# Kernel optimization log

Hardware: AMD Instinct MI355X
Metric: run time of the kernel (lower is better)

Reference implementation:

```python
import math
import jax, jax.numpy as jnp
import numpy as np

# ---- static hyperparams (match init_kwargs) ----
B, D, K, NC, F = 16384, 64, 128, 64, 256
TAU_MIN = 0.01
TAU_DENOM_MIN = 0.001
EPS = 0.001  # transport_eps


def setup_inputs() -> dict:
    key = jax.random.key(0)
    ks = jax.random.split(key, 8)
    # latent positions strictly inside the Poincare ball (norm < 0.9)
    z = jax.random.normal(ks[0], (B, D), jnp.float32)
    z = z / (jnp.linalg.norm(z, axis=-1, keepdims=True) + 1e-6)
    z = z * (0.9 * jax.random.uniform(ks[1], (B, 1), jnp.float32))
    features = jax.random.normal(ks[2], (B, F), jnp.float32)
    q_z_w = jax.random.normal(ks[3], (K, D), jnp.float32) * 0.02
    q_z_b = jnp.zeros((K,), jnp.float32)
    q_feat_w = jax.random.normal(ks[4], (K, F), jnp.float32) * 0.02
    q_feat_b = jnp.zeros((K,), jnp.float32)
    q_gamma = jax.random.normal(ks[5], (K, D, D), jnp.float32) * 0.02
    chart_queries = jax.random.normal(ks[6], (NC, K), jnp.float32) * 0.02
    return {"z": z, "features": features, "q_z_w": q_z_w, "q_z_b": q_z_b,
            "q_feat_w": q_feat_w, "q_feat_b": q_feat_b, "q_gamma": q_gamma,
            "chart_queries": chart_queries}


def _hyperbolic_score(z, centers):
    # z: [B, D]; centers: [NC, D] -> scores [B, NC]
    diff = z[:, None, :] - centers[None, :, :]
    dist_sq = (diff ** 2).sum(-1)                       # [B, NC]
    z_sq = (z ** 2).sum(-1, keepdims=True)              # [B, 1]
    c_sq = (centers ** 2).sum(-1)[None, :]              # [1, NC]
    denom = (1.0 - z_sq) * (1.0 - c_sq)
    arg = 1.0 + 2.0 * dist_sq / (denom + EPS)
    dist = jnp.arccosh(jnp.maximum(arg, 1.0 + EPS))
    # metric-aware temperature tau(z)
    tau = math.sqrt(K) * jnp.maximum(1.0 - z_sq[:, 0], TAU_DENOM_MIN) / 2.0
    tau = jnp.maximum(tau, TAU_MIN)                     # [B]
    return -dist / tau[:, None]


def reference(z, features, q_z_w, q_z_b, q_feat_w, q_feat_b, q_gamma, chart_queries):
    # chart centers live in the first D coords of the chart queries
    centers = chart_queries[:, :D]                      # [NC, D]
    scores = _hyperbolic_score(z, centers)              # [B, NC]

    # query: linear(z) + linear(features) + bilinear gamma term
    q = z @ q_z_w.T + q_z_b + features @ q_feat_w.T + q_feat_b   # [B, K]
    q = q + jnp.einsum("bi,bj,kij->bk", z, z, q_gamma)           # gamma contraction

    # O(n) hyperbolic parallel transport: scale queries by 1/lambda(z)
    r2 = jnp.minimum((z ** 2).sum(-1, keepdims=True), 1.0 - EPS)  # [B, 1]
    lam = 2.0 / (1.0 - r2 + EPS)                                  # [B, 1]
    tq = chart_queries[None, :, :] / lam[:, None, :]              # [B, NC, K]

    scores = scores + jnp.einsum("bk,bnk->bn", q, tq) / math.sqrt(K)
    weights = jax.nn.softmax(scores, axis=-1)           # [B, NC] (soft routing)
    k_chart = jnp.argmax(weights, axis=-1)              # [B]
    return weights, k_chart
```

## Files before the change

### kernel.cpp

```cpp
#include <hip/hip_runtime.h>
#include <hip/hip_bf16.h>
#include <cmath>
#include <cstring>

#define B_TOT 16384

typedef unsigned int uint_t;
typedef unsigned short ushort_t;
typedef __attribute__((ext_vector_type(8))) short bf16x8;
typedef __attribute__((ext_vector_type(16))) float f32x16;

#define WS_TAB 0
#define WS_CSQ 1024
#define WS_LIN 4096
#define WS_S   4198400
#define WS_PPK 5246976

__global__ __launch_bounds__(256) void prep_s(const float* __restrict__ g,
                                              const float* __restrict__ cq,
                                              char* __restrict__ ws) {
  __shared__ float gl[128][68];
  __shared__ float cql[16][132];
  float* S = (float*)(ws + WS_S);
  const int ns = blockIdx.x >> 6, J = blockIdx.x & 63, t = threadIdx.x;
  for (int i = t; i < 2048; i += 256) {
    const int k = i >> 4, c4 = (i & 15) * 4;
    *(float4*)&gl[k][c4] = *(const float4*)(g + (size_t)k * 4096 + J * 64 + c4);
  }
  for (int i = t; i < 2048; i += 256) {
    const int n16 = i >> 7, k = i & 127;
    cql[n16][k] = cq[(ns * 16 + n16) * 128 + k];
  }
  __syncthreads();
  const int n16 = t >> 4, c4 = (t & 15) * 4;
  float4 acc = {0.f, 0.f, 0.f, 0.f};
#pragma unroll 8
  for (int k = 0; k < 128; ++k) {
    const float w = cql[n16][k];
    const float4 gv = *(const float4*)&gl[k][c4];
    acc.x = fmaf(w, gv.x, acc.x);
    acc.y = fmaf(w, gv.y, acc.y);
    acc.z = fmaf(w, gv.z, acc.z);
    acc.w = fmaf(w, gv.w, acc.w);
  }
  *(float4*)(S + (size_t)(ns * 16 + n16) * 4096 + J * 64 + c4) = acc;
}

__global__ __launch_bounds__(256) void prep_pack(
    const float* __restrict__ qfw, const float* __restrict__ cq,
    const float* __restrict__ qzw, const float* __restrict__ qzb,
    const float* __restrict__ qfb, char* __restrict__ ws) {
  __shared__ float Sl[4096];
  __shared__ uint_t tabl[192];
  __shared__ float psumf[128][2];
  const int n = blockIdx.x & 63, part = blockIdx.x >> 6, t = threadIdx.x;
  const float* __restrict__ S = (const float*)(ws + WS_S) + (size_t)n * 4096;
  for (int i = t; i < 4096; i += 256) Sl[i] = S[i];
  if (t < 64) {
    const int i = t;
    const int start = (i < 16) ? 4 * i
                     : (i < 32) ? 64 + 3 * (i - 16)
                     : (i < 48) ? 112 + 2 * (i - 32)
                                : 144 + (i - 48);
    const int nst = 4 - (i >> 4);
    for (int u = 0; u < nst; ++u)
      tabl[start + u] = (0u << 16) | ((uint_t)i << 8) | (uint_t)(16 * ((i >> 4) + u));
  } else if (t < 80) tabl[160 + (t - 64)] = (1u << 16) | (uint_t)((t - 64) * 16);
  else if (t < 84)   tabl[176 + (t - 80)] = (2u << 16) | (uint_t)((t - 80) * 16);
  else if (t == 84)  tabl[180] = (3u << 16);
  else if (t < 96)   tabl[181 + (t - 85)] = 0;
  __syncthreads();
  if (part == 0 && n == 0 && t < 192) ((uint_t*)(ws + WS_TAB))[t] = tabl[t];

  const int mt = n >> 5, r = n & 31;
  auto wpack = [&](int s, int jo, float val) {
    const __hip_bfloat16 hb = __float2bfloat16(val);
    const float hf = __bfloat162float(hb);
    const __hip_bfloat16 lb = __float2bfloat16(val - hf);
    ushort_t hu, lu;
    memcpy(&hu, &hb, 2);
    memcpy(&lu, &lb, 2);
    const size_t base =
        (((size_t)s * 4 + mt * 2) * 64 + ((jo >> 3) & 1) * 32 + r) * 16 + (jo & 7) * 2;
    *(ushort_t*)(ws + WS_PPK + base) = hu;
    *(ushort_t*)(ws + WS_PPK + base + 1024) = lu;
  };

  for (int v = part * 640 + t; v < (part + 1) * 640; v += 256) {
    const int s = v >> 4, jo = v & 15;
    const uint_t inf = tabl[s];
    const int i = (inf >> 8) & 255, j0 = inf & 255;
    const int j = j0 + jo;
    const float val =
        (j < i) ? 0.f : ((j > i) ? Sl[i * 64 + j] + Sl[j * 64 + i] : Sl[i * 64 + i]);
    wpack(s, jo, val);
  }
  const float* __restrict__ cqn = cq + n * 128;

  if (part >= 2) {
    const int fl = t & 127, kh = t >> 7;
    const int f = (part - 2) * 128 + fl;
    float a = 0.f;
#pragma unroll 8
    for (int k = 0; k < 64; ++k)
      a = fmaf(qfw[(kh * 64 + k) * 256 + f], cqn[kh * 64 + k], a);
    psumf[fl][kh] = a;
    __syncthreads();
    if (t < 128) {
      const int ff = (part - 2) * 128 + t;
      wpack(160 + (ff >> 4), ff & 15, psumf[t][0] + psumf[t][1]);
    }
  } else if (part == 1) {
    if (t < 64) {
      float a = 0.f;
#pragma unroll 8
      for (int k = 0; k < 128; ++k) a = fmaf(cqn[k], qzw[k * 64 + t], a);
      wpack(176 + (t >> 4), t & 15, a);
    }
    for (int v2 = t; v2 < 176; v2 += 256) wpack(181 + (v2 >> 4), v2 & 15, 0.f);
  } else {
    if (t == 128) {
      float a = 0.f;
      for (int k = 0; k < 128; ++k) a = fmaf(qzb[k] + qfb[k], cqn[k], a);
      wpack(180, 0, a);
    } else if (t > 128 && t < 144) wpack(180, t - 128, 0.f);
    if (t == 144) {
      double a = 0.0;
      for (int d = 0; d < 64; ++d) a = fma((double)cqn[d], (double)cqn[d], a);
      ((double*)(ws + WS_CSQ))[n] = a;
    }
  }
}

__global__ __launch_bounds__(256, 4) void gemm_tail_kernel(
    const float* __restrict__ z, const float* __restrict__ feat,
    const float* __restrict__ cq, char* __restrict__ ws,
    float* __restrict__ out) {
  __shared__ __align__(16) unsigned char smem[46208];
  float (*z_lds)[68] = (float (*)[68])(smem);
  float (*s_lin)[65] = (float (*)[65])(smem + 8704);
  float (*zt)[33] = (float (*)[33])(smem + 17024);
  float (*cqT)[65] = (float (*)[65])(smem + 25472);
  double (*s_exp)[65] = (double (*)[65])(smem + 25472);
  double (*pmax)[9] = (double (*)[9])(smem + 42112);
  int (*parg)[9] = (int (*)[9])(smem + 44416);
  double* rowmax = (double*)(smem + 45568);
  int* rowarg = (int*)(smem + 45824);
  double* rowinv = (double*)(smem + 45952);

  const int t = threadIdx.x, lane = t & 63;
  const int wv = __builtin_amdgcn_readfirstlane(t >> 6);
  const int b0 = blockIdx.x * 32;
  const int h = lane >> 5, c = lane & 31;

  for (int i = t; i < 2048; i += 256) z_lds[i >> 6][i & 63] = z[(size_t)b0 * 64 + i];
  if (t < 128) z_lds[t >> 2][64 + (t & 3)] = 0.f;
  for (int i = t; i < 32 * 65; i += 256) ((float*)s_lin)[i] = 0.f;
  __syncthreads();

  const bf16x8* __restrict__ pp = (const bf16x8*)(ws + WS_PPK);
  const uint_t* __restrict__ tab = (const uint_t*)(ws + WS_TAB);
  f32x16 acc[2] = {};
#pragma unroll 2
  for (int it = 0; it < 46; ++it) {
    const int s = wv + it * 4;
    const uint_t inf = tab[s];
    const int mode = inf >> 16, i_idx = (inf >> 8) & 255, p0 = inf & 255;
    const bf16x8 Ah0 = pp[((size_t)s * 4 + 0) * 64 + lane];
    const bf16x8 Al0 = pp[((size_t)s * 4 + 1) * 64 + lane];
    const bf16x8 Ah1 = pp[((size_t)s * 4 + 2) * 64 + lane];
    const bf16x8 Al1 = pp[((size_t)s * 4 + 3) * 64 + lane];
    const int bl = c;
    float xv[8];
    if (mode == 0) {
      const float zi = z_lds[bl][i_idx];
      const float* __restrict__ zp = &z_lds[bl][p0 + h * 8];
      const float4 a = *(const float4*)zp, b2 = *(const float4*)(zp + 4);
      xv[0] = zi * a.x; xv[1] = zi * a.y; xv[2] = zi * a.z; xv[3] = zi * a.w;
      xv[4] = zi * b2.x; xv[5] = zi * b2.y; xv[6] = zi * b2.z; xv[7] = zi * b2.w;
    } else if (mode == 1) {
      const float* __restrict__ fp = feat + (size_t)(b0 + bl) * 256 + p0 + h * 8;
      const float4 a = *(const float4*)fp, b2 = *(const float4*)(fp + 4);
      xv[0] = a.x; xv[1] = a.y; xv[2] = a.z; xv[3] = a.w;
      xv[4] = b2.x; xv[5] = b2.y; xv[6] = b2.z; xv[7] = b2.w;
    } else if (mode == 2) {
      const float* __restrict__ zp = &z_lds[bl][p0 + h * 8];
      const float4 a = *(const float4*)zp, b2 = *(const float4*)(zp + 4);
      xv[0] = a.x; xv[1] = a.y; xv[2] = a.z; xv[3] = a.w;
      xv[4] = b2.x; xv[5] = b2.y; xv[6] = b2.z; xv[7] = b2.w;
    } else {
      xv[0] = (h == 0) ? 1.f : 0.f;
      xv[1] = xv[2] = xv[3] = xv[4] = xv[5] = xv[6] = xv[7] = 0.f;
    }
    uint_t bhw[4], blw[4];
#pragma unroll
    for (int e2 = 0; e2 < 4; ++e2) {
      const float2 xp = {xv[2 * e2], xv[2 * e2 + 1]};
      const __hip_bfloat162 hb2 = __float22bfloat162_rn(xp);
      uint_t hw;
      memcpy(&hw, &hb2, 4);
      const float h0 = __uint_as_float(hw << 16);
      const float h1 = __uint_as_float(hw & 0xffff0000u);
      const float2 lp = {xp.x - h0, xp.y - h1};
      const __hip_bfloat162 lb2 = __float22bfloat162_rn(lp);
      uint_t lw;
      memcpy(&lw, &lb2, 4);
      bhw[e2] = hw;
      blw[e2] = lw;
    }
    bf16x8 Bh, Bl;
    memcpy(&Bh, bhw, 16);
    memcpy(&Bl, blw, 16);
    acc[0] = __builtin_amdgcn_mfma_f32_32x32x16_bf16(Ah0, Bh, acc[0], 0, 0, 0);
    acc[0] = __builtin_amdgcn_mfma_f32_32x32x16_bf16(Ah0, Bl, acc[0], 0, 0, 0);
    acc[0] = __builtin_amdgcn_mfma_f32_32x32x16_bf16(Al0, Bh, acc[0], 0, 0, 0);
    acc[1] = __builtin_amdgcn_mfma_f32_32x32x16_bf16(Ah1, Bh, acc[1], 0, 0, 0);
    acc[1] = __builtin_amdgcn_mfma_f32_32x32x16_bf16(Ah1, Bl, acc[1], 0, 0, 0);
    acc[1] = __builtin_amdgcn_mfma_f32_32x32x16_bf16(Al1, Bh, acc[1], 0, 0, 0);
  }
#pragma unroll
  for (int mt = 0; mt < 2; ++mt)
#pragma unroll
    for (int r = 0; r < 16; ++r) {
      const int n = mt * 32 + (r & 3) + 8 * (r >> 2) + 4 * h;
      atomicAdd(&s_lin[c][n], acc[mt][r]);
    }

  for (int i = t; i < 2048; i += 256) zt[i & 63][i >> 6] = z[(size_t)b0 * 64 + i];
  for (int i = t; i < 4096; i += 256) {
    const int n = i >> 6, ii = i & 63;
    cqT[ii][n] = cq[n * 128 + ii];
  }
  __syncthreads();

  const int r = t & 31, cg = t >> 5;

  double z_sq = 0.0, zc[8] = {0.0, 0.0, 0.0, 0.0, 0.0, 0.0, 0.0, 0.0};
#pragma unroll 4
  for (int i = 0; i < 64; ++i) {
    const double zv = (double)zt[i][r];
    z_sq = fma(zv, zv, z_sq);
#pragma unroll
    for (int u = 0; u < 8; ++u)
      zc[u] = fma(zv, (double)cqT[i][cg + 8 * u], zc[u]);
  }
  float lin[8];
#pragma unroll
  for (int u = 0; u < 8; ++u) lin[u] = s_lin[r][cg + 8 * u];

  const double EPS = 0.001;
  const double SQRTK = sqrt(128.0);
  double tau = SQRTK * fmax(1.0 - z_sq, 0.001) * 0.5;
  tau = fmax(tau, 0.01);
  const double inv_tau = 1.0 / tau;
  const double r2 = fmin(z_sq, 1.0 - EPS);
  const double lam_fac = (1.0 - r2 + EPS) * 0.5 / SQRTK;
  const double* __restrict__ csqd = (const double*)(ws + WS_CSQ);

  double sc[8];
#pragma unroll
  for (int u = 0; u < 8; ++u) {
    const int n = cg + 8 * u;
    const double c_sq = csqd[n];
    const double dist_sq = z_sq + c_sq - 2.0 * zc[u];
    const double denom = (1.0 - z_sq) * (1.0 - c_sq);
    double arg = 1.0 + 2.0 * dist_sq / (denom + EPS);
    arg = fmax(arg, 1.0 + EPS);
    const double dist = log(arg + sqrt(arg * arg - 1.0));
    sc[u] = -dist * inv_tau + (double)lin[u] * lam_fac;
  }
  __syncthreads();

  {
    double mx = sc[0];
    int am = cg;
#pragma unroll
    for (int u = 1; u < 8; ++u)
      if (sc[u] > mx) { mx = sc[u]; am = cg + 8 * u; }
    pmax[r][cg] = mx;
    parg[r][cg] = am;
  }
  __syncthreads();
  if (t < 32) {
    double m = pmax[t][0];
    int a = parg[t][0];
#pragma unroll
    for (int g = 1; g < 8; ++g) {
      const double v = pmax[t][g];
      const int aa = parg[t][g];
      if (v > m || (v == m && aa < a)) { m = v; a = aa; }
    }
    rowmax[t] = m;
    rowarg[t] = a;
  }
  __syncthreads();
  {
    const double m = rowmax[r];
    double ps = 0.0;
#pragma unroll
    for (int u = 0; u < 8; ++u) {
      const double e = exp(sc[u] - m);
      s_exp[r][cg + 8 * u] = e;
      ps += e;
    }
    pmax[r][cg] = ps;
  }
  __syncthreads();
  if (t < 32) {
    double s = 0.0;
#pragma unroll
    for (int g = 0; g < 8; ++g) s += pmax[t][g];
    rowinv[t] = 1.0 / s;
  }
  __syncthreads();
  for (int idx = t; idx < 2048; idx += 256) {
    const int b = idx >> 6, n = idx & 63;
    out[(size_t)(b0 + b) * 64 + n] = (float)(s_exp[b][n] * rowinv[b]);
  }
  if (t < 32) out[(size_t)B_TOT * 64 + b0 + t] = (float)rowarg[t];
}

extern "C" void kernel_launch(void* const* d_in, const int* in_sizes, int n_in,
                              void* d_out, int out_size, void* d_ws, size_t ws_size,
                              hipStream_t stream) {
  const float* z = (const float*)d_in[0];
  const float* feat = (const float*)d_in[1];
  const float* qzw = (const float*)d_in[2];
  const float* qzb = (const float*)d_in[3];
  const float* qfw = (const float*)d_in[4];
  const float* qfb = (const float*)d_in[5];
  const float* gamma = (const float*)d_in[6];
  const float* cq = (const float*)d_in[7];
  float* out = (float*)d_out;
  char* ws = (char*)d_ws;

  prep_s<<<dim3(256), dim3(256), 0, stream>>>(gamma, cq, ws);
  prep_pack<<<dim3(256), dim3(256), 0, stream>>>(qfw, cq, qzw, qzb, qfb, ws);
  gemm_tail_kernel<<<dim3(B_TOT / 32), dim3(256), 0, stream>>>(z, feat, cq, ws, out);
}
```

Before: 154.0 us.

## Use six waves per block and prefetch next step's packed weights

The GEMM kernel grows from 4 to 6 waves per block, so the 184 K-steps split as 32 per wave instead of 46, and the step table is staged in LDS. Each iteration now issues loads for the next step's A fragments and table entry before the current MFMAs, software-pipelining global latency. The extra two waves sit idle in the tail epilogue, and occupancy per CU may drop because of the new launch bounds and the registers held by prefetching.

```diff
diff --git a/kernel.cpp b/kernel.cpp
--- a/kernel.cpp
+++ b/kernel.cpp
@@ -132,11 +132,11 @@
   }
 }
 
-__global__ __launch_bounds__(256, 4) void gemm_tail_kernel(
+__global__ __launch_bounds__(384, 3) void gemm_tail_kernel(
     const float* __restrict__ z, const float* __restrict__ feat,
     const float* __restrict__ cq, char* __restrict__ ws,
     float* __restrict__ out) {
-  __shared__ __align__(16) unsigned char smem[46208];
+  __shared__ __align__(16) unsigned char smem[46976];
   float (*z_lds)[68] = (float (*)[68])(smem);
   float (*s_lin)[65] = (float (*)[65])(smem + 8704);
   float (*zt)[33] = (float (*)[33])(smem + 17024);
@@ -147,29 +147,37 @@
   double* rowmax = (double*)(smem + 45568);
   int* rowarg = (int*)(smem + 45824);
   double* rowinv = (double*)(smem + 45952);
+  uint_t* tab_lds = (uint_t*)(smem + 46208);
 
   const int t = threadIdx.x, lane = t & 63;
   const int wv = __builtin_amdgcn_readfirstlane(t >> 6);
   const int b0 = blockIdx.x * 32;
   const int h = lane >> 5, c = lane & 31;
 
-  for (int i = t; i < 2048; i += 256) z_lds[i >> 6][i & 63] = z[(size_t)b0 * 64 + i];
+  for (int i = t; i < 2048; i += 384) z_lds[i >> 6][i & 63] = z[(size_t)b0 * 64 + i];
   if (t < 128) z_lds[t >> 2][64 + (t & 3)] = 0.f;
-  for (int i = t; i < 32 * 65; i += 256) ((float*)s_lin)[i] = 0.f;
+  for (int i = t; i < 32 * 65; i += 384) ((float*)s_lin)[i] = 0.f;
+  if (t < 192) tab_lds[t] = ((const uint_t*)(ws + WS_TAB))[t];
   __syncthreads();
 
   const bf16x8* __restrict__ pp = (const bf16x8*)(ws + WS_PPK);
-  const uint_t* __restrict__ tab = (const uint_t*)(ws + WS_TAB);
   f32x16 acc[2] = {};
+  int s = wv;
+  uint_t inf = tab_lds[s];
+  bf16x8 Ah0 = pp[((size_t)s * 4 + 0) * 64 + lane];
+  bf16x8 Al0 = pp[((size_t)s * 4 + 1) * 64 + lane];
+  bf16x8 Ah1 = pp[((size_t)s * 4 + 2) * 64 + lane];
+  bf16x8 Al1 = pp[((size_t)s * 4 + 3) * 64 + lane];
 #pragma unroll 2
-  for (int it = 0; it < 46; ++it) {
-    const int s = wv + it * 4;
-    const uint_t inf = tab[s];
+  for (int it = 0; it < 32; ++it) {
+    const int sn = (it < 31) ? (s + 6) : s;
+    const bf16x8 nAh0 = pp[((size_t)sn * 4 + 0) * 64 + lane];
+    const bf16x8 nAl0 = pp[((size_t)sn * 4 + 1) * 64 + lane];
+    const bf16x8 nAh1 = pp[((size_t)sn * 4 + 2) * 64 + lane];
+    const bf16x8 nAl1 = pp[((size_t)sn * 4 + 3) * 64 + lane];
+    const uint_t ninf = tab_lds[sn];
+
     const int mode = inf >> 16, i_idx = (inf >> 8) & 255, p0 = inf & 255;
-    const bf16x8 Ah0 = pp[((size_t)s * 4 + 0) * 64 + lane];
-    const bf16x8 Al0 = pp[((size_t)s * 4 + 1) * 64 + lane];
-    const bf16x8 Ah1 = pp[((size_t)s * 4 + 2) * 64 + lane];
-    const bf16x8 Al1 = pp[((size_t)s * 4 + 3) * 64 + lane];
     const int bl = c;
     float xv[8];
     if (mode == 0) {
@@ -217,6 +225,9 @@
     acc[1] = __builtin_amdgcn_mfma_f32_32x32x16_bf16(Ah1, Bh, acc[1], 0, 0, 0);
     acc[1] = __builtin_amdgcn_mfma_f32_32x32x16_bf16(Ah1, Bl, acc[1], 0, 0, 0);
     acc[1] = __builtin_amdgcn_mfma_f32_32x32x16_bf16(Al1, Bh, acc[1], 0, 0, 0);
+
+    Ah0 = nAh0; Al0 = nAl0; Ah1 = nAh1; Al1 = nAl1;
+    inf = ninf; s = sn;
   }
 #pragma unroll
   for (int mt = 0; mt < 2; ++mt)
@@ -226,52 +237,54 @@
       atomicAdd(&s_lin[c][n], acc[mt][r]);
     }
 
-  for (int i = t; i < 2048; i += 256) zt[i & 63][i >> 6] = z[(size_t)b0 * 64 + i];
-  for (int i = t; i < 4096; i += 256) {
+  for (int i = t; i < 2048; i += 384) zt[i & 63][i >> 6] = z[(size_t)b0 * 64 + i];
+  for (int i = t; i < 4096; i += 384) {
     const int n = i >> 6, ii = i & 63;
     cqT[ii][n] = cq[n * 128 + ii];
   }
   __syncthreads();
 
   const int r = t & 31, cg = t >> 5;
-
-  double z_sq = 0.0, zc[8] = {0.0, 0.0, 0.0, 0.0, 0.0, 0.0, 0.0, 0.0};
+  const double EPS = 0.001;
+  double sc[8];
+
+  if (cg < 8) {
+    double z_sq = 0.0, zc[8] = {0.0, 0.0, 0.0, 0.0, 0.0, 0.0, 0.0, 0.0};
 #pragma unroll 4
-  for (int i = 0; i < 64; ++i) {
-    const double zv = (double)zt[i][r];
-    z_sq = fma(zv, zv, z_sq);
-#pragma unroll
-    for (int u = 0; u < 8; ++u)
-      zc[u] = fma(zv, (double)cqT[i][cg + 8 * u], zc[u]);
-  }
-  float lin[8];
-#pragma unroll
-  for (int u = 0; u < 8; ++u) lin[u] = s_lin[r][cg + 8 * u];
-
-  const double EPS = 0.001;
-  const double SQRTK = sqrt(128.0);
-  double tau = SQRTK * fmax(1.0 - z_sq, 0.001) * 0.5;
-  tau = fmax(tau, 0.01);
-  const double inv_tau = 1.0 / tau;
-  const double r2 = fmin(z_sq, 1.0 - EPS);
-  const double lam_fac = (1.0 - r2 + EPS) * 0.5 / SQRTK;
-  const double* __restrict__ csqd = (const double*)(ws + WS_CSQ);
-
-  double sc[8];
-#pragma unroll
-  for (int u = 0; u < 8; ++u) {
-    const int n = cg + 8 * u;
-    const double c_sq = csqd[n];
-    const double dist_sq = z_sq + c_sq - 2.0 * zc[u];
-    const double denom = (1.0 - z_sq) * (1.0 - c_sq);
-    double arg = 1.0 + 2.0 * dist_sq / (denom + EPS);
-    arg = fmax(arg, 1.0 + EPS);
-    const double dist = log(arg + sqrt(arg * arg - 1.0));
-    sc[u] = -dist * inv_tau + (double)lin[u] * lam_fac;
-  }
-  __syncthreads();
-
-  {
+    for (int i = 0; i < 64; ++i) {
+      const double zv = (double)zt[i][r];
+      z_sq = fma(zv, zv, z_sq);
+#pragma unroll
+      for (int u = 0; u < 8; ++u)
+        zc[u] = fma(zv, (double)cqT[i][cg + 8 * u], zc[u]);
+    }
+    float lin[8];
+#pragma unroll
+    for (int u = 0; u < 8; ++u) lin[u] = s_lin[r][cg + 8 * u];
+
+    const double SQRTK = sqrt(128.0);
+    double tau = SQRTK * fmax(1.0 - z_sq, 0.001) * 0.5;
+    tau = fmax(tau, 0.01);
+    const double inv_tau = 1.0 / tau;
+    const double r2 = fmin(z_sq, 1.0 - EPS);
+    const double lam_fac = (1.0 - r2 + EPS) * 0.5 / SQRTK;
+    const double* __restrict__ csqd = (const double*)(ws + WS_CSQ);
+
+#pragma unroll
+    for (int u = 0; u < 8; ++u) {
+      const int n = cg + 8 * u;
+      const double c_sq = csqd[n];
+      const double dist_sq = z_sq + c_sq - 2.0 * zc[u];
+      const double denom = (1.0 - z_sq) * (1.0 - c_sq);
+      double arg = 1.0 + 2.0 * dist_sq / (denom + EPS);
+      arg = fmax(arg, 1.0 + EPS);
+      const double dist = log(arg + sqrt(arg * arg - 1.0));
+      sc[u] = -dist * inv_tau + (double)lin[u] * lam_fac;
+    }
+  }
+  __syncthreads();
+
+  if (cg < 8) {
     double mx = sc[0];
     int am = cg;
 #pragma unroll
@@ -294,7 +307,7 @@
     rowarg[t] = a;
   }
   __syncthreads();
-  {
+  if (cg < 8) {
     const double m = rowmax[r];
     double ps = 0.0;
 #pragma unroll
@@ -307,13 +320,13 @@
   }
   __syncthreads();
   if (t < 32) {
-    double s = 0.0;
-#pragma unroll
-    for (int g = 0; g < 8; ++g) s += pmax[t][g];
-    rowinv[t] = 1.0 / s;
-  }
-  __syncthreads();
-  for (int idx = t; idx < 2048; idx += 256) {
+    double s2 = 0.0;
+#pragma unroll
+    for (int g = 0; g < 8; ++g) s2 += pmax[t][g];
+    rowinv[t] = 1.0 / s2;
+  }
+  __syncthreads();
+  for (int idx = t; idx < 2048; idx += 384) {
     const int b = idx >> 6, n = idx & 63;
     out[(size_t)(b0 + b) * 64 + n] = (float)(s_exp[b][n] * rowinv[b]);
   }
@@ -336,5 +349,5 @@
 
   prep_s<<<dim3(256), dim3(256), 0, stream>>>(gamma, cq, ws);
   prep_pack<<<dim3(256), dim3(256), 0, stream>>>(qfw, cq, qzw, qzb, qfb, ws);
-  gemm_tail_kernel<<<dim3(B_TOT / 32), dim3(256), 0, stream>>>(z, feat, cq, ws, out);
+  gemm_tail_kernel<<<dim3(B_TOT / 32), dim3(384), 0, stream>>>(z, feat, cq, ws, out);
 }
```

Measured after the change: 166.0 us. 7.8% more time.
